# Performance work log

Measured on AMD Instinct MI355X. Metric: run time of the kernel, lower is better.

## Reference

```python
import jax, jax.numpy as jnp
import numpy as np

N, C_IN, H, W = 48, 64, 128, 128


def _conv3x3(x, w, b):
    # NCHW conv, kernel 3, stride 1, pad 1 (SAME)
    y = jax.lax.conv_general_dilated(
        x, w, window_strides=(1, 1), padding=((1, 1), (1, 1)),
        dimension_numbers=("NCHW", "OIHW", "NCHW"))
    return y + b[None, :, None, None]


def setup_inputs() -> dict:
    key = jax.random.key(0)
    ks = jax.random.split(key, 4)
    s1 = 1.0 / np.sqrt(C_IN * 9)
    s2 = 1.0 / np.sqrt(128 * 9)
    s3 = 1.0 / np.sqrt(32 * 9)
    return {
        "x": jax.random.normal(ks[0], (N, C_IN, H, W), dtype=jnp.float32),
        "to_process": jnp.arange(N, dtype=jnp.int64) if jax.config.jax_enable_x64 else jnp.arange(N, dtype=jnp.int32),
        "batch_size": 8,
        "W1": jax.random.normal(ks[1], (128, C_IN, 3, 3), dtype=jnp.float32) * s1,
        "b1": jnp.zeros((128,), dtype=jnp.float32),
        "W2": jax.random.normal(ks[2], (32, 128, 3, 3), dtype=jnp.float32) * s2,
        "b2": jnp.zeros((32,), dtype=jnp.float32),
        "W3": jax.random.normal(ks[3], (1, 32, 3, 3), dtype=jnp.float32) * s3,
        "b3": jnp.zeros((1,), dtype=jnp.float32),
    }


def reference(x, to_process, batch_size, W1, b1, W2, b2, W3, b3):
    # x holds only the active sites listed in to_process; all ops are per-site.
    x = jax.nn.relu(_conv3x3(x, W1, b1))          # [N,128,H,W]
    x = jax.nn.relu(_conv3x3(x, W2, b2))          # [N,32,H,W]
    n, c, h, w = x.shape
    # SparseBilinearUpsample(2): half-pixel-center bilinear x2 (align_corners=False)
    x = jax.image.resize(x, (n, c, 2 * h, 2 * w), method="bilinear")
    x = _conv3x3(x, W3, b3)                        # [N,1,2H,2W]
    return x
```

## Files before the change

### kernel.cpp

```cpp
#include <hip/hip_runtime.h>


typedef _Float16 half_t;
typedef _Float16 half2_t __attribute__((ext_vector_type(2)));
typedef _Float16 half4_t __attribute__((ext_vector_type(4)));
typedef _Float16 half8   __attribute__((ext_vector_type(8)));
typedef float    floatx4  __attribute__((ext_vector_type(4)));
typedef float    floatx16 __attribute__((ext_vector_type(16)));

__global__ __launch_bounds__(256) void repack_w(
    const float* __restrict__ W1, const float* __restrict__ W2,
    const float* __restrict__ W3, half_t* __restrict__ wh1,
    half_t* __restrict__ wh2, half_t* __restrict__ wh3)
{
    int idx = blockIdx.x * 256 + threadIdx.x;
    if (idx < 73728) {
        int ci = idx & 63, co = (idx >> 6) & 127, tap = idx >> 13;
        wh1[idx] = (half_t)W1[(co * 64 + ci) * 9 + tap];
    } else if (idx < 110592) {
        int j = idx - 73728;
        int ci = j & 127, co = (j >> 7) & 31, tap = j >> 12;
        wh2[j] = (half_t)W2[(co * 128 + ci) * 9 + tap];
    } else if (idx < 110880) {
        int j = idx - 110592;
        int ci = j & 31, tap = j >> 5;
        wh3[j] = (half_t)W3[ci * 9 + tap];
    }
}

__global__ __launch_bounds__(256) void repack_x(
    const float* __restrict__ x, half_t* __restrict__ xh)
{
    const int tid = threadIdx.x;
    const int px = tid & 127, rr = tid >> 7;
    const int y = blockIdx.x * 2 + rr;
    const int n = blockIdx.y;
    const float* xn = x + (size_t)n * 64 * 16384 + (size_t)y * 128 + px;
    half2_t hb[32];
#pragma unroll
    for (int c2 = 0; c2 < 32; ++c2) {
        float f0 = xn[(size_t)(2 * c2) * 16384];
        float f1 = xn[(size_t)(2 * c2 + 1) * 16384];
        half2_t h; h.x = (half_t)f0; h.y = (half_t)f1;
        hb[c2] = h;
    }
    half_t* op = xh + (((size_t)n * 128 + y) * 128 + px) * 64;
#pragma unroll
    for (int k = 0; k < 8; ++k)
        *(half8*)(op + k * 8) = *(half8*)(&hb[k * 4]);
}

__global__ __launch_bounds__(256, 2) void conv1_mfma(
    const half_t* __restrict__ xh,
    const half_t* __restrict__ wh,
    const float*  __restrict__ bias,
    half_t* __restrict__ y1h)
{
    __shared__ half_t lx[10 * 34 * 72];
    const int tid  = threadIdx.x;
    const int lane = tid & 63;
    const int wave = tid >> 6;
    const int l31 = lane & 31, lq = lane >> 5;
    const int wco = wave >> 1, wpx = wave & 1;
    const int x0 = blockIdx.x * 32, y0 = blockIdx.y * 8;
    const int n = blockIdx.z;
    const half_t* xn = xh + (size_t)n * (128 * 128 * 64);

    half8 st[11];
#pragma unroll
    for (int k = 0; k < 11; ++k) {
        int idx = tid + k * 256;
        half8 v = {};
        if (idx < 10 * 34 * 8) {
            int ch = idx & 7;
            int p  = idx >> 3;
            int col = p % 34, row = p / 34;
            int gx = x0 - 1 + col, gy = y0 - 1 + row;
            if ((unsigned)gx < 128u && (unsigned)gy < 128u)
                v = *(const half8*)(xn + ((size_t)gy * 128 + gx) * 64 + ch * 8);
        }
        st[k] = v;
    }
#pragma unroll
    for (int k = 0; k < 11; ++k) {
        int idx = tid + k * 256;
        if (idx < 10 * 34 * 8) {
            int ch = idx & 7;
            int p  = idx >> 3;
            int col = p % 34, row = p / 34;
            *(half8*)(&lx[(row * 34 + col) * 72 + ch * 8]) = st[k];
        }
    }
    __syncthreads();

    floatx16 acc[2][4] = {};

#pragma unroll
    for (int tap = 0; tap < 9; ++tap) {
        const int dy = tap / 3, dx = tap % 3;
        const half_t* wt = wh + tap * (128 * 64) + (wco * 64 + l31) * 64 + lq * 8;
        const half_t* bp = &lx[((wpx * 4 + dy) * 34 + l31 + dx) * 72 + lq * 8];
#pragma unroll
        for (int kc = 0; kc < 4; ++kc) {
            half8 a0 = *(const half8*)(wt + kc * 16);
            half8 a1 = *(const half8*)(wt + 32 * 64 + kc * 16);
            half8 b[4];
#pragma unroll
            for (int nf = 0; nf < 4; ++nf)
                b[nf] = *(const half8*)(bp + nf * (34 * 72) + kc * 16);
#pragma unroll
            for (int nf = 0; nf < 4; ++nf) {
                acc[0][nf] = __builtin_amdgcn_mfma_f32_32x32x16_f16(a0, b[nf], acc[0][nf], 0, 0, 0);
                acc[1][nf] = __builtin_amdgcn_mfma_f32_32x32x16_f16(a1, b[nf], acc[1][nf], 0, 0, 0);
            }
        }
    }

#pragma unroll
    for (int mf = 0; mf < 2; ++mf) {
        int co0 = wco * 64 + mf * 32 + lq * 4;
#pragma unroll
        for (int nf = 0; nf < 4; ++nf) {
            floatx16 A = acc[mf][nf];
            int oy = y0 + wpx * 4 + nf, ox = x0 + l31;
            half_t* op = y1h + (((size_t)n * 128 + oy) * 128 + ox) * 128 + co0;
#pragma unroll
            for (int g = 0; g < 4; ++g) {
                floatx4 bv = *(const floatx4*)(bias + co0 + 8 * g);
                half4_t o;
                o.x = (half_t)fmaxf(A[4 * g + 0] + bv.x, 0.f);
                o.y = (half_t)fmaxf(A[4 * g + 1] + bv.y, 0.f);
                o.z = (half_t)fmaxf(A[4 * g + 2] + bv.z, 0.f);
                o.w = (half_t)fmaxf(A[4 * g + 3] + bv.w, 0.f);
                *(half4_t*)(op + 8 * g) = o;
            }
        }
    }
}

__global__ __launch_bounds__(256, 3) void conv2_mfma(
    const half_t* __restrict__ y1h,
    const half_t* __restrict__ wh,
    const float*  __restrict__ bias,
    half_t* __restrict__ y2h)
{
    __shared__ half_t lx[18 * 34 * 40];
    const int tid  = threadIdx.x;
    const int lane = tid & 63;
    const int w    = tid >> 6;
    const int l15 = lane & 15, quad = lane >> 4;
    const int x0 = blockIdx.x * 32, y0 = blockIdx.y * 16;
    const int n = blockIdx.z;
    const half_t* yn = y1h + (size_t)n * (128 * 128 * 128);

    floatx4 acc[2][8] = {};

    for (int h = 0; h < 4; ++h) {
        for (int idx = tid; idx < 18 * 34 * 4; idx += 256) {
            int ch = idx & 3;
            int col = (idx >> 2) % 34;
            int row = (idx >> 2) / 34;
            int gx = x0 - 1 + col, gy = y0 - 1 + row;
            half8 v = {};
            if ((unsigned)gx < 128u && (unsigned)gy < 128u)
                v = *(const half8*)(yn + ((size_t)gy * 128 + gx) * 128 + h * 32 + ch * 8);
            *(half8*)(&lx[(row * 34 + col) * 40 + ch * 8]) = v;
        }
        __syncthreads();
#pragma unroll
        for (int tap = 0; tap < 9; ++tap) {
            const int dy = tap / 3, dx = tap % 3;
            const half_t* wt = wh + tap * (32 * 128) + l15 * 128 + h * 32 + quad * 8;
            half8 a0 = *(const half8*)(wt);
            half8 a1 = *(const half8*)(wt + 16 * 128);
#pragma unroll
            for (int nf = 0; nf < 8; ++nf) {
                int rr = w * 4 + (nf >> 1) + dy;
                int cc = (nf & 1) * 16 + l15 + dx;
                half8 b = *(const half8*)(&lx[(rr * 34 + cc) * 40 + quad * 8]);
                acc[0][nf] = __builtin_amdgcn_mfma_f32_16x16x32_f16(a0, b, acc[0][nf], 0, 0, 0);
                acc[1][nf] = __builtin_amdgcn_mfma_f32_16x16x32_f16(a1, b, acc[1][nf], 0, 0, 0);
            }
        }
        __syncthreads();
    }

#pragma unroll
    for (int mf = 0; mf < 2; ++mf) {
        int co0 = mf * 16 + quad * 4;
        floatx4 bv = *(const floatx4*)(bias + co0);
#pragma unroll
        for (int nf = 0; nf < 8; ++nf) {
            int oy = y0 + w * 4 + (nf >> 1), ox = x0 + (nf & 1) * 16 + l15;
            floatx4 A = acc[mf][nf];
            half4_t o;
            o.x = (half_t)fmaxf(A.x + bv.x, 0.f);
            o.y = (half_t)fmaxf(A.y + bv.y, 0.f);
            o.z = (half_t)fmaxf(A.z + bv.z, 0.f);
            o.w = (half_t)fmaxf(A.w + bv.w, 0.f);
            *(half4_t*)(y2h + (((size_t)n * 128 + oy) * 128 + ox) * 32 + co0) = o;
        }
    }
}

__global__ __launch_bounds__(256) void conv3_fused(
    const half_t* __restrict__ y2h,
    const half_t* __restrict__ wh3,
    const float*  __restrict__ bias,
    float* __restrict__ out)
{
    __shared__ half_t lu[10 * 34 * 40];
    const int tid = threadIdx.x;
    const int c = tid & 31, r = tid >> 5;
    const int x0 = blockIdx.x * 32, y0 = blockIdx.y * 8;
    const int n = blockIdx.z;
    const half_t* base = y2h + (size_t)n * (128 * 128 * 32);

    for (int idx = tid; idx < 10 * 34 * 4; idx += 256) {
        int cc = idx & 3;
        int p  = idx >> 2;
        int col = p % 34, row = p / 34;
        int X = x0 - 1 + col, Y = y0 - 1 + row;
        half8 o = {};
        if ((unsigned)X < 256u && (unsigned)Y < 256u) {
            int jx = X >> 1, jy = Y >> 1;
            int jxo = (X & 1) ? (jx < 127 ? jx + 1 : 127) : (jx > 0 ? jx - 1 : 0);
            int jyo = (Y & 1) ? (jy < 127 ? jy + 1 : 127) : (jy > 0 ? jy - 1 : 0);
            const half_t* p00 = base + ((size_t)jy  * 128 + jx ) * 32 + cc * 8;
            const half_t* p01 = base + ((size_t)jy  * 128 + jxo) * 32 + cc * 8;
            const half_t* p10 = base + ((size_t)jyo * 128 + jx ) * 32 + cc * 8;
            const half_t* p11 = base + ((size_t)jyo * 128 + jxo) * 32 + cc * 8;
            half8 v00 = *(const half8*)p00;
            half8 v01 = *(const half8*)p01;
            half8 v10 = *(const half8*)p10;
            half8 v11 = *(const half8*)p11;
            o = v00 * (half_t)0.5625f + (v01 + v10) * (half_t)0.1875f
              + v11 * (half_t)0.0625f;
        }
        *(half8*)(&lu[(row * 34 + col) * 40 + cc * 8]) = o;
    }
    __syncthreads();

    float acc = 0.f;
#pragma unroll
    for (int tap = 0; tap < 9; ++tap) {
        const int dy = tap / 3, dx = tap % 3;
        const half_t* lp = &lu[((r + dy) * 34 + c + dx) * 40];
        const half_t* wp = wh3 + tap * 32;
#pragma unroll
        for (int cc = 0; cc < 4; ++cc) {
            half8 v = *(const half8*)(lp + cc * 8);
            half8 w = *(const half8*)(wp + cc * 8);
            acc = __builtin_amdgcn_fdot2(__builtin_shufflevector(v, v, 0, 1),
                                         __builtin_shufflevector(w, w, 0, 1), acc, false);
            acc = __builtin_amdgcn_fdot2(__builtin_shufflevector(v, v, 2, 3),
                                         __builtin_shufflevector(w, w, 2, 3), acc, false);
            acc = __builtin_amdgcn_fdot2(__builtin_shufflevector(v, v, 4, 5),
                                         __builtin_shufflevector(w, w, 4, 5), acc, false);
            acc = __builtin_amdgcn_fdot2(__builtin_shufflevector(v, v, 6, 7),
                                         __builtin_shufflevector(w, w, 6, 7), acc, false);
        }
    }
    out[((size_t)n * 256 + (y0 + r)) * 256 + x0 + c] = acc + bias[0];
}

extern "C" void kernel_launch(void* const* d_in, const int* in_sizes, int n_in,
                              void* d_out, int out_size, void* d_ws, size_t ws_size,
                              hipStream_t stream) {
    const float* x  = (const float*)d_in[0];
    const float* W1 = (const float*)d_in[3];
    const float* b1 = (const float*)d_in[4];
    const float* W2 = (const float*)d_in[5];
    const float* b2 = (const float*)d_in[6];
    const float* W3 = (const float*)d_in[7];
    const float* b3 = (const float*)d_in[8];
    float* out = (float*)d_out;

    char* ws = (char*)d_ws;
    half_t* xh  = (half_t*)ws;
    half_t* y1h = (half_t*)(ws + 201326592ull);
    half_t* y2h = (half_t*)(ws + 402653184ull);
    half_t* wh1 = (half_t*)(ws + 452984832ull);
    half_t* wh2 = wh1 + 73728;
    half_t* wh3 = wh2 + 36864;

    repack_w<<<434, 256, 0, stream>>>(W1, W2, W3, wh1, wh2, wh3);
    repack_x<<<dim3(64, 48), 256, 0, stream>>>(x, xh);
    conv1_mfma<<<dim3(4, 16, 48), 256, 0, stream>>>(xh, wh1, b1, y1h);
    conv2_mfma<<<dim3(4, 8, 48), 256, 0, stream>>>(y1h, wh2, b2, y2h);
    conv3_fused<<<dim3(8, 32, 48), 256, 0, stream>>>(y2h, wh3, b3, out);
}
```

Before: 741.3 us.

## Double-buffer conv1 input tiles by channel halves and process two row tiles per block

```diff
diff --git a/kernel.cpp b/kernel.cpp
--- a/kernel.cpp
+++ b/kernel.cpp
@@ -56,83 +56,114 @@
     const float*  __restrict__ bias,
     half_t* __restrict__ y1h)
 {
-    __shared__ half_t lx[10 * 34 * 72];
+    __shared__ half_t lx[2][10 * 34 * 36];
     const int tid  = threadIdx.x;
     const int lane = tid & 63;
     const int wave = tid >> 6;
     const int l31 = lane & 31, lq = lane >> 5;
     const int wco = wave >> 1, wpx = wave & 1;
-    const int x0 = blockIdx.x * 32, y0 = blockIdx.y * 8;
+    const int x0 = blockIdx.x * 32;
+    const int ybase = blockIdx.y * 16;
     const int n = blockIdx.z;
     const half_t* xn = xh + (size_t)n * (128 * 128 * 64);
 
-    half8 st[11];
-#pragma unroll
-    for (int k = 0; k < 11; ++k) {
+    half8 st[6];
+
+#pragma unroll
+    for (int k = 0; k < 6; ++k) {
         int idx = tid + k * 256;
         half8 v = {};
-        if (idx < 10 * 34 * 8) {
-            int ch = idx & 7;
-            int p  = idx >> 3;
+        if (idx < 1360) {
+            int ch = idx & 3;
+            int p  = idx >> 2;
             int col = p % 34, row = p / 34;
-            int gx = x0 - 1 + col, gy = y0 - 1 + row;
+            int gx = x0 - 1 + col, gy = ybase - 1 + row;
             if ((unsigned)gx < 128u && (unsigned)gy < 128u)
                 v = *(const half8*)(xn + ((size_t)gy * 128 + gx) * 64 + ch * 8);
         }
         st[k] = v;
     }
-#pragma unroll
-    for (int k = 0; k < 11; ++k) {
-        int idx = tid + k * 256;
-        if (idx < 10 * 34 * 8) {
-            int ch = idx & 7;
-            int p  = idx >> 3;
-            int col = p % 34, row = p / 34;
-            *(half8*)(&lx[(row * 34 + col) * 72 + ch * 8]) = st[k];
-        }
-    }
-    __syncthreads();
-
-    floatx16 acc[2][4] = {};
-
-#pragma unroll
-    for (int tap = 0; tap < 9; ++tap) {
-        const int dy = tap / 3, dx = tap % 3;
-        const half_t* wt = wh + tap * (128 * 64) + (wco * 64 + l31) * 64 + lq * 8;
-        const half_t* bp = &lx[((wpx * 4 + dy) * 34 + l31 + dx) * 72 + lq * 8];
-#pragma unroll
-        for (int kc = 0; kc < 4; ++kc) {
-            half8 a0 = *(const half8*)(wt + kc * 16);
-            half8 a1 = *(const half8*)(wt + 32 * 64 + kc * 16);
-            half8 b[4];
-#pragma unroll
-            for (int nf = 0; nf < 4; ++nf)
-                b[nf] = *(const half8*)(bp + nf * (34 * 72) + kc * 16);
+
+#pragma unroll
+    for (int t = 0; t < 2; ++t) {
+        const int y0 = ybase + t * 8;
+        floatx16 acc[2][4] = {};
+#pragma unroll
+        for (int h = 0; h < 2; ++h) {
+            const int q = t * 2 + h;
+            const int buf = q & 1;
+
+#pragma unroll
+            for (int k = 0; k < 6; ++k) {
+                int idx = tid + k * 256;
+                if (idx < 1360) {
+                    int ch = idx & 3;
+                    int p  = idx >> 2;
+                    int col = p % 34, row = p / 34;
+                    *(half8*)(&lx[buf][(row * 34 + col) * 36 + ch * 8]) = st[k];
+                }
+            }
+            __syncthreads();
+
+            if (q < 3) {
+                const int tn = (q + 1) >> 1, hn = (q + 1) & 1;
+                const int y0n = ybase + tn * 8;
+#pragma unroll
+                for (int k = 0; k < 6; ++k) {
+                    int idx = tid + k * 256;
+                    half8 v = {};
+                    if (idx < 1360) {
+                        int ch = idx & 3;
+                        int p  = idx >> 2;
+                        int col = p % 34, row = p / 34;
+                        int gx = x0 - 1 + col, gy = y0n - 1 + row;
+                        if ((unsigned)gx < 128u && (unsigned)gy < 128u)
+                            v = *(const half8*)(xn + ((size_t)gy * 128 + gx) * 64 + hn * 32 + ch * 8);
+                    }
+                    st[k] = v;
+                }
+            }
+
+#pragma unroll
+            for (int tap = 0; tap < 9; ++tap) {
+                const int dy = tap / 3, dx = tap % 3;
+                const half_t* wt = wh + tap * (128 * 64) + (wco * 64 + l31) * 64 + h * 32 + lq * 8;
+                const half_t* bp = &lx[buf][((wpx * 4 + dy) * 34 + l31 + dx) * 36 + lq * 8];
+#pragma unroll
+                for (int kc = 0; kc < 2; ++kc) {
+                    half8 a0 = *(const half8*)(wt + kc * 16);
+                    half8 a1 = *(const half8*)(wt + 32 * 64 + kc * 16);
+                    half8 b[4];
+#pragma unroll
+                    for (int nf = 0; nf < 4; ++nf)
+                        b[nf] = *(const half8*)(bp + nf * (34 * 36) + kc * 16);
+#pragma unroll
+                    for (int nf = 0; nf < 4; ++nf) {
+                        acc[0][nf] = __builtin_amdgcn_mfma_f32_32x32x16_f16(a0, b[nf], acc[0][nf], 0, 0, 0);
+                        acc[1][nf] = __builtin_amdgcn_mfma_f32_32x32x16_f16(a1, b[nf], acc[1][nf], 0, 0, 0);
+                    }
+                }
+            }
+        }
+
+#pragma unroll
+        for (int mf = 0; mf < 2; ++mf) {
+            int co0 = wco * 64 + mf * 32 + lq * 4;
 #pragma unroll
             for (int nf = 0; nf < 4; ++nf) {
-                acc[0][nf] = __builtin_amdgcn_mfma_f32_32x32x16_f16(a0, b[nf], acc[0][nf], 0, 0, 0);
-                acc[1][nf] = __builtin_amdgcn_mfma_f32_32x32x16_f16(a1, b[nf], acc[1][nf], 0, 0, 0);
-            }
-        }
-    }
-
-#pragma unroll
-    for (int mf = 0; mf < 2; ++mf) {
-        int co0 = wco * 64 + mf * 32 + lq * 4;
-#pragma unroll
-        for (int nf = 0; nf < 4; ++nf) {
-            floatx16 A = acc[mf][nf];
-            int oy = y0 + wpx * 4 + nf, ox = x0 + l31;
-            half_t* op = y1h + (((size_t)n * 128 + oy) * 128 + ox) * 128 + co0;
-#pragma unroll
-            for (int g = 0; g < 4; ++g) {
-                floatx4 bv = *(const floatx4*)(bias + co0 + 8 * g);
-                half4_t o;
-                o.x = (half_t)fmaxf(A[4 * g + 0] + bv.x, 0.f);
-                o.y = (half_t)fmaxf(A[4 * g + 1] + bv.y, 0.f);
-                o.z = (half_t)fmaxf(A[4 * g + 2] + bv.z, 0.f);
-                o.w = (half_t)fmaxf(A[4 * g + 3] + bv.w, 0.f);
-                *(half4_t*)(op + 8 * g) = o;
+                floatx16 A = acc[mf][nf];
+                int oy = y0 + wpx * 4 + nf, ox = x0 + l31;
+                half_t* op = y1h + (((size_t)n * 128 + oy) * 128 + ox) * 128 + co0;
+#pragma unroll
+                for (int g = 0; g < 4; ++g) {
+                    floatx4 bv = *(const floatx4*)(bias + co0 + 8 * g);
+                    half4_t o;
+                    o.x = (half_t)fmaxf(A[4 * g + 0] + bv.x, 0.f);
+                    o.y = (half_t)fmaxf(A[4 * g + 1] + bv.y, 0.f);
+                    o.z = (half_t)fmaxf(A[4 * g + 2] + bv.z, 0.f);
+                    o.w = (half_t)fmaxf(A[4 * g + 3] + bv.w, 0.f);
+                    *(half4_t*)(op + 8 * g) = o;
+                }
             }
         }
     }
@@ -286,7 +317,7 @@
 
     repack_w<<<434, 256, 0, stream>>>(W1, W2, W3, wh1, wh2, wh3);
     repack_x<<<dim3(64, 48), 256, 0, stream>>>(x, xh);
-    conv1_mfma<<<dim3(4, 16, 48), 256, 0, stream>>>(xh, wh1, b1, y1h);
+    conv1_mfma<<<dim3(4, 8, 48), 256, 0, stream>>>(xh, wh1, b1, y1h);
     conv2_mfma<<<dim3(4, 8, 48), 256, 0, stream>>>(y1h, wh2, b2, y2h);
     conv3_fused<<<dim3(8, 32, 48), 256, 0, stream>>>(y2h, wh3, b3, out);
 }
```

New measurement: 810.3 us. 1.09x slower.
